# Kernel tuning notes

Measured on AMD Instinct MI355X. Metric: run time of the kernel, lower is better.

The kernel has to match this reference:

```python
import jax, jax.numpy as jnp
import numpy as np

N = 50000   # nodes
E = 800000  # edges (before self-loops)
G = 512     # graphs in batch
H = 4       # heads
C = 32      # hidden dim per head
NEG = 0.2   # LeakyReLU slope in GATConv
EPS = 1e-5  # BatchNorm eps


def setup_inputs():
    k = jax.random.split(jax.random.key(0), 32)
    f = lambda i, s: 0.1 * jax.random.normal(k[i], s, dtype=jnp.float32)
    inp = {
        "x": jax.random.normal(k[0], (N, 4), dtype=jnp.float32),
        "edge_index": jax.random.randint(k[1], (2, E), 0, N, dtype=jnp.int32),
        "batch": ((jnp.arange(N) * G) // N).astype(jnp.int32),  # sorted, every graph non-empty
        "u": jax.random.normal(k[2], (G, 10), dtype=jnp.float32),
    }
    dims = [(4, H * C, H, H * C), (H * C, H * C, H, H * C), (H * C, C, 1, C)]
    j = 3
    for l, (din, dout, hh, dbn) in enumerate(dims):
        inp[f"W{l}"] = f(j, (din, dout)); j += 1
        inp[f"a_src{l}"] = f(j, (hh, C)); j += 1
        inp[f"a_dst{l}"] = f(j, (hh, C)); j += 1
        inp[f"b{l}"] = f(j, (dbn,)); j += 1
        inp[f"bn_g{l}"] = 1.0 + f(j, (dbn,)); j += 1
        inp[f"bn_b{l}"] = f(j, (dbn,)); j += 1
        inp[f"bn_m{l}"] = f(j, (dbn,)); j += 1
        inp[f"bn_v{l}"] = 1.0 + 0.1 * jax.random.uniform(k[j], (dbn,), dtype=jnp.float32); j += 1
    inp["l1w"] = f(j, (2 * C + 10, C)); j += 1
    inp["l1b"] = f(j, (C,)); j += 1
    inp["l2w"] = f(j, (C, 1)); j += 1
    inp["l2b"] = f(j, (1,)); j += 1
    return inp


def gat(x, src, dst, W, a_s, a_d, b, heads, ch, concat):
    n = x.shape[0]
    h = (x @ W).reshape(n, heads, ch)                                   # [N,H,C]
    al_s = jnp.einsum('nhc,hc->nh', h, a_s)
    al_d = jnp.einsum('nhc,hc->nh', h, a_d)
    e = jax.nn.leaky_relu(al_s[src] + al_d[dst], NEG)                   # [E',H]
    m = jax.ops.segment_max(e, dst, num_segments=n)                     # per-dst softmax
    p = jnp.exp(e - m[dst])
    alpha = p / (jax.ops.segment_sum(p, dst, num_segments=n)[dst] + 1e-16)
    out = jax.ops.segment_sum(h[src] * alpha[:, :, None], dst, num_segments=n)
    out = out.reshape(n, heads * ch) if concat else out.mean(axis=1)
    return out + b


def bn(x, g, b, m, v):  # eval-mode BatchNorm1d
    return (x - m) * jax.lax.rsqrt(v + EPS) * g + b


def reference(x, edge_index, batch, u,
              W0, a_src0, a_dst0, b0, bn_g0, bn_b0, bn_m0, bn_v0,
              W1, a_src1, a_dst1, b1, bn_g1, bn_b1, bn_m1, bn_v1,
              W2, a_src2, a_dst2, b2, bn_g2, bn_b2, bn_m2, bn_v2,
              l1w, l1b, l2w, l2b):
    loops = jnp.arange(N, dtype=edge_index.dtype)  # GATConv add_self_loops=True
    src = jnp.concatenate([edge_index[0], loops])
    dst = jnp.concatenate([edge_index[1], loops])
    x = jax.nn.elu(bn(gat(x, src, dst, W0, a_src0, a_dst0, b0, H, C, True), bn_g0, bn_b0, bn_m0, bn_v0))
    x = jax.nn.elu(bn(gat(x, src, dst, W1, a_src1, a_dst1, b1, H, C, True), bn_g1, bn_b1, bn_m1, bn_v1))
    x = jax.nn.elu(bn(gat(x, src, dst, W2, a_src2, a_dst2, b2, 1, C, False), bn_g2, bn_b2, bn_m2, bn_v2))
    cnt = jax.ops.segment_sum(jnp.ones((N,), x.dtype), batch, num_segments=G)
    x_mean = jax.ops.segment_sum(x, batch, num_segments=G) / cnt[:, None]
    x_max = jax.ops.segment_max(x, batch, num_segments=G)
    comb = jnp.concatenate([x_mean, x_max, u], axis=1)                  # [G, 2C+10]
    hid = jax.nn.relu(comb @ l1w + l1b)
    return jax.nn.sigmoid(hid @ l2w + l2b)[:, 0]                        # [G]
```

## Files before the change

### kernel.cpp

```cpp
#include <hip/hip_runtime.h>
#include <hip/hip_bf16.h>
#include <math.h>

#define LRELU_NEG 0.2f
#define BN_EPS 1e-5f
#define CSR_SHIFT 7

typedef __attribute__((ext_vector_type(8))) short bf16x8;
typedef __attribute__((ext_vector_type(4))) float f32x4;

__device__ __forceinline__ float lrelu(float x) { return x > 0.f ? x : LRELU_NEG * x; }
__device__ __forceinline__ float b2f(__hip_bfloat16 v) { return __bfloat162float(v); }
__device__ __forceinline__ unsigned short f2bu(float v) {
  __hip_bfloat16 b = __float2bfloat16(v);
  return *(unsigned short*)&b;
}
__device__ __forceinline__ float blo(unsigned int u) { return __uint_as_float(u << 16); }
__device__ __forceinline__ float bhi(unsigned int u) { return __uint_as_float(u & 0xFFFF0000u); }
__device__ __forceinline__ float elu_fast(float v) { return v > 0.f ? v : __expf(v) - 1.f; }

__global__ __launch_bounds__(256) void k_detect(const unsigned short* __restrict__ w, int n,
                                                int* __restrict__ flag, int* __restrict__ ghist) {
  __shared__ int bad_s;
  int tid = threadIdx.x;
  ghist[tid] = 0; ghist[tid + 256] = 0;
  if (tid == 0) bad_s = 0;
  __syncthreads();
  int bad = 0;
  for (int i = 2 * tid; i < n; i += 512) {
    unsigned short u = w[i];
    if ((u & 0x7FFF) == 0) continue;
    int ex = (u >> 7) & 0xFF;
    if (ex > 131 || ex < 90) bad++;
  }
  atomicAdd(&bad_s, bad);
  __syncthreads();
  if (tid == 0) *flag = (bad_s < 2048) ? 1 : 0;
}

struct CvtArgs {
  const void* src[30];
  float* dst[30];
  int n[30];
};

__global__ __launch_bounds__(256) void k_cvt_all(CvtArgs a, const int* __restrict__ flag) {
  int ai = blockIdx.y;
  int n = a.n[ai];
  int i = blockIdx.x * 256 + threadIdx.x;
  if (i >= n) return;
  if (*flag) {
    a.dst[ai][i] = b2f(((const __hip_bfloat16*)a.src[ai])[i]);
  } else {
    a.dst[ai][i] = ((const float*)a.src[ai])[i];
  }
}

__global__ __launch_bounds__(256) void k_foldW(const float* __restrict__ W0, const float* __restrict__ as0, const float* __restrict__ ad0,
                                               const float* __restrict__ W1, const float* __restrict__ as1, const float* __restrict__ ad1,
                                               const float* __restrict__ W2, const float* __restrict__ as2, const float* __restrict__ ad2,
                                               float* __restrict__ W0p, __hip_bfloat16* __restrict__ Wt1, __hip_bfloat16* __restrict__ Wt2) {
  int idx = blockIdx.x * 256 + threadIdx.x;
  if (idx < 576) {
    int k = idx / 144, c = idx % 144;
    float v = 0.f;
    if (c < 128) v = W0[k * 128 + c];
    else if (c < 136) {
      int hh = (c - 128) & 3; const float* a = (c < 132) ? as0 : ad0;
      float s = 0.f;
      for (int cc = 0; cc < 32; cc++) s += W0[k * 128 + hh * 32 + cc] * a[hh * 32 + cc];
      v = s;
    }
    W0p[k * 144 + c] = v;
    return;
  }
  idx -= 576;
  if (idx < 144 * 128) {
    int c = idx >> 7, k = idx & 127;
    float v = 0.f;
    if (c < 128) v = W1[k * 128 + c];
    else if (c < 136) {
      int hh = (c - 128) & 3; const float* a = (c < 132) ? as1 : ad1;
      float s = 0.f;
      for (int cc = 0; cc < 32; cc++) s += W1[k * 128 + hh * 32 + cc] * a[hh * 32 + cc];
      v = s;
    }
    Wt1[c * 128 + k] = __float2bfloat16(v);
    return;
  }
  idx -= 144 * 128;
  if (idx < 48 * 128) {
    int c = idx >> 7, k = idx & 127;
    float v = 0.f;
    if (c < 32) v = W2[k * 32 + c];
    else if (c == 32) { float s = 0.f; for (int cc = 0; cc < 32; cc++) s += W2[k * 32 + cc] * as2[cc]; v = s; }
    else if (c == 33) { float s = 0.f; for (int cc = 0; cc < 32; cc++) s += W2[k * 32 + cc] * ad2[cc]; v = s; }
    Wt2[c * 128 + k] = __float2bfloat16(v);
  }
}

__global__ __launch_bounds__(256) void k_binhist(const int* __restrict__ ei, int* __restrict__ ghist,
                                                 int E, int EN) {
  __shared__ int hist[512];
  int tid = threadIdx.x;
  hist[tid] = 0; hist[tid + 256] = 0;
  __syncthreads();
  int base = blockIdx.x * 4096;
  for (int i = 0; i < 16; i++) {
    int e = base + i * 256 + tid;
    if (e < EN) {
      int dst = (e < E) ? ei[E + e] : (e - E);
      atomicAdd(&hist[dst >> CSR_SHIFT], 1);
    }
  }
  __syncthreads();
  if (hist[tid]) atomicAdd(&ghist[tid], hist[tid]);
  if (hist[tid + 256]) atomicAdd(&ghist[tid + 256], hist[tid + 256]);
}

__global__ __launch_bounds__(512) void k_bucketscan(const int* __restrict__ ghist,
                                                    int* __restrict__ bbase, int* __restrict__ gcursor) {
  __shared__ int wpre[8];
  int tid = threadIdx.x, lane = tid & 63, wid = tid >> 6;
  int v = ghist[tid];
  int x = v;
  #pragma unroll
  for (int off = 1; off < 64; off <<= 1) {
    int y = __shfl_up(x, off);
    if (lane >= off) x += y;
  }
  if (lane == 63) wpre[wid] = x;
  __syncthreads();
  if (tid == 0) {
    int acc = 0;
    #pragma unroll
    for (int w = 0; w < 8; w++) { int t = wpre[w]; wpre[w] = acc; acc += t; }
  }
  __syncthreads();
  int excl = wpre[wid] + x - v;
  bbase[tid] = excl;
  gcursor[tid] = excl;
  if (tid == 511) bbase[512] = excl + v;
}

__global__ __launch_bounds__(256) void k_binscatter(const int* __restrict__ ei, int* __restrict__ gcursor,
                                                    unsigned int* __restrict__ pairs, int E, int EN) {
  __shared__ int cnt[512];
  __shared__ int base[512];
  int tid = threadIdx.x;
  cnt[tid] = 0; cnt[tid + 256] = 0;
  __syncthreads();
  int eb = blockIdx.x * 4096;
  int srcs[16], dsts[16];
  #pragma unroll
  for (int i = 0; i < 16; i++) {
    int e = eb + i * 256 + tid;
    srcs[i] = -1; dsts[i] = 0;
    if (e < EN) {
      int s, d;
      if (e < E) { s = ei[e]; d = ei[E + e]; } else { s = e - E; d = s; }
      srcs[i] = s; dsts[i] = d;
      atomicAdd(&cnt[d >> CSR_SHIFT], 1);
    }
  }
  __syncthreads();
  for (int b = tid; b < 512; b += 256) {
    int c = cnt[b];
    base[b] = c ? atomicAdd(&gcursor[b], c) : 0;
    cnt[b] = 0;
  }
  __syncthreads();
  #pragma unroll
  for (int i = 0; i < 16; i++) {
    if (srcs[i] >= 0) {
      int b = dsts[i] >> CSR_SHIFT;
      int loc = atomicAdd(&cnt[b], 1);
      pairs[base[b] + loc] = ((unsigned int)srcs[i] << CSR_SHIFT) | (unsigned int)(dsts[i] & 127);
    }
  }
}

__global__ __launch_bounds__(256) void k_csrfin(const unsigned int* __restrict__ pairs,
                                                const int* __restrict__ bbase,
                                                int* __restrict__ rs, int* __restrict__ col,
                                                int N, int EN) {
  __shared__ int dcount[128];
  __shared__ int wsum;
  __shared__ int lcur[128];
  int b = blockIdx.x, tid = threadIdx.x;
  if (tid < 128) dcount[tid] = 0;
  __syncthreads();
  int s = bbase[b], e = bbase[b + 1];
  for (int i = s + tid; i < e; i += 256)
    atomicAdd(&dcount[pairs[i] & 127], 1);
  __syncthreads();
  int x = 0, v = 0, wid = 0;
  if (tid < 128) {
    v = dcount[tid];
    int lane = tid & 63; wid = tid >> 6;
    x = v;
    #pragma unroll
    for (int off = 1; off < 64; off <<= 1) {
      int y = __shfl_up(x, off);
      if (lane >= off) x += y;
    }
    if (wid == 0 && lane == 63) wsum = x;
  }
  __syncthreads();
  if (tid < 128) {
    int excl = x - v + (wid ? wsum : 0);
    int r = s + excl;
    int node = (b << CSR_SHIFT) + tid;
    if (node < N) rs[node] = r;
    lcur[tid] = r;
  }
  if (b == 0 && tid == 0) rs[N] = EN;
  __syncthreads();
  for (int i = s + tid; i < e; i += 256) {
    unsigned int p = pairs[i];
    int pos = atomicAdd(&lcur[p & 127], 1);
    col[pos] = (int)(p >> CSR_SHIFT);
  }
}

__global__ __launch_bounds__(256) void k_gemm0(const float* __restrict__ x, const float* __restrict__ W0p,
    __hip_bfloat16* __restrict__ h, float* __restrict__ als, float* __restrict__ ald, int N) {
  int t = blockIdx.x * 256 + threadIdx.x;
  int nrow = t / 36, cg = t - nrow * 36;
  if (nrow >= N) return;
  float4 xv = *(const float4*)(x + (size_t)nrow * 4);
  int c0 = cg * 4;
  float o[4];
  #pragma unroll
  for (int j = 0; j < 4; j++) {
    int c = c0 + j;
    o[j] = fmaf(xv.x, W0p[c], fmaf(xv.y, W0p[144 + c], fmaf(xv.z, W0p[288 + c], xv.w * W0p[432 + c])));
  }
  if (c0 < 128) {
    uint2 pk;
    pk.x = ((unsigned int)f2bu(o[1]) << 16) | f2bu(o[0]);
    pk.y = ((unsigned int)f2bu(o[3]) << 16) | f2bu(o[2]);
    *((uint2*)((unsigned short*)h + (size_t)nrow * 128) + cg) = pk;
  } else if (c0 == 128) {
    *(float4*)(als + (size_t)nrow * 4) = make_float4(o[0], o[1], o[2], o[3]);
  } else {
    *(float4*)(ald + (size_t)nrow * 4) = make_float4(o[0], o[1], o[2], o[3]);
  }
}

template <int CT, int DOUT, int HEADS>
__global__ __launch_bounds__(256) void k_mm(const __hip_bfloat16* __restrict__ xa,
    const __hip_bfloat16* __restrict__ Wt,
    __hip_bfloat16* __restrict__ h, float* __restrict__ als, float* __restrict__ ald, int N) {
  __shared__ unsigned short A_s[64 * 128];
  __shared__ unsigned short B_s[CT * 16 * 128];
  int tid = threadIdx.x;
  int row0 = blockIdx.x * 64;

  for (int i = tid; i < 1024; i += 256) {
    int r = i >> 4, slot = i & 15;
    int gr = row0 + r;
    float4 v = make_float4(0.f, 0.f, 0.f, 0.f);
    if (gr < N) v = ((const float4*)(xa + (size_t)gr * 128))[slot];
    *(float4*)((char*)A_s + r * 256 + ((slot ^ (r & 7)) << 4)) = v;
  }
  for (int i = tid; i < CT * 256; i += 256) {
    int r = i >> 4, slot = i & 15;
    float4 v = ((const float4*)Wt)[i];
    *(float4*)((char*)B_s + r * 256 + ((slot ^ (r & 7)) << 4)) = v;
  }
  __syncthreads();

  int l = tid & 63, w = tid >> 6;
  int lr = l & 15, lg = l >> 4;
  f32x4 acc[CT];
  #pragma unroll
  for (int ct = 0; ct < CT; ct++) acc[ct] = (f32x4){0.f, 0.f, 0.f, 0.f};

  int rA = w * 16 + lr;
  #pragma unroll
  for (int k0 = 0; k0 < 4; k0++) {
    int slot = k0 * 4 + lg;
    bf16x8 a = *(const bf16x8*)((const char*)A_s + rA * 256 + ((slot ^ (rA & 7)) << 4));
    #pragma unroll
    for (int ct = 0; ct < CT; ct++) {
      int rB = ct * 16 + lr;
      bf16x8 b = *(const bf16x8*)((const char*)B_s + rB * 256 + ((slot ^ (rB & 7)) << 4));
      acc[ct] = __builtin_amdgcn_mfma_f32_16x16x32_bf16(a, b, acc[ct], 0, 0, 0);
    }
  }

  #pragma unroll
  for (int ct = 0; ct < CT; ct++) {
    #pragma unroll
    for (int j = 0; j < 4; j++) {
      int gr = row0 + w * 16 + lg * 4 + j;
      if (gr >= N) continue;
      int col = ct * 16 + lr;
      float v = acc[ct][j];
      if (col < DOUT)                 h[(size_t)gr * DOUT + col] = __float2bfloat16(v);
      else if (col < DOUT + HEADS)    als[(size_t)gr * HEADS + (col - DOUT)] = v;
      else if (col < DOUT + 2*HEADS)  ald[(size_t)gr * HEADS + (col - DOUT - HEADS)] = v;
    }
  }
}

__global__ __launch_bounds__(256) void k_agg4(const __hip_bfloat16* __restrict__ h, const float* __restrict__ als,
    const float* __restrict__ ald, const int* __restrict__ rs, const int* __restrict__ col,
    const float* __restrict__ bias, const float* __restrict__ bng,
    const float* __restrict__ bnb, const float* __restrict__ bnm,
    const float* __restrict__ bnv, __hip_bfloat16* __restrict__ out, int N) {
  __shared__ int svs[8][32];
  __shared__ float ps[8][32][4];
  int tid = threadIdx.x;
  int sub = tid & 31, gi = tid >> 5;
  int n = blockIdx.x * 8 + gi;
  if (n >= N) return;
  int row = rs[n], deg = rs[n + 1] - row;
  float4 ad4 = *(const float4*)(ald + (size_t)n * 4);
  int hh2 = sub >> 3;
  float acc0 = 0.f, acc1 = 0.f, acc2 = 0.f, acc3 = 0.f;
  float s0 = 0.f, s1 = 0.f, s2 = 0.f, s3 = 0.f;

  for (int base = 0; base < deg; base += 32) {
    int k = base + sub;
    int sv = 0; float q0 = 0.f, q1 = 0.f, q2 = 0.f, q3 = 0.f;
    if (k < deg) {
      sv = col[row + k];
      float4 a4 = *(const float4*)(als + (size_t)sv * 4);
      q0 = __expf(lrelu(a4.x + ad4.x));
      q1 = __expf(lrelu(a4.y + ad4.y));
      q2 = __expf(lrelu(a4.z + ad4.z));
      q3 = __expf(lrelu(a4.w + ad4.w));
    }
    svs[gi][sub] = sv;
    *(float4*)&ps[gi][sub][0] = make_float4(q0, q1, q2, q3);
    s0 += q0; s1 += q1; s2 += q2; s3 += q3;
    int cnt = min(32, deg - base);
    int e = 0;
    for (; e + 3 < cnt; e += 4) {
      float pA = ps[gi][e][hh2];     int sA = svs[gi][e];
      float pB = ps[gi][e + 1][hh2]; int sB = svs[gi][e + 1];
      float pC = ps[gi][e + 2][hh2]; int sC = svs[gi][e + 2];
      float pD = ps[gi][e + 3][hh2]; int sD = svs[gi][e + 3];
      uint2 hA = *((const uint2*)(h + (size_t)sA * 128) + sub);
      uint2 hB = *((const uint2*)(h + (size_t)sB * 128) + sub);
      uint2 hC = *((const uint2*)(h + (size_t)sC * 128) + sub);
      uint2 hD = *((const uint2*)(h + (size_t)sD * 128) + sub);
      acc0 = fmaf(pA, blo(hA.x), acc0); acc1 = fmaf(pA, bhi(hA.x), acc1);
      acc2 = fmaf(pA, blo(hA.y), acc2); acc3 = fmaf(pA, bhi(hA.y), acc3);
      acc0 = fmaf(pB, blo(hB.x), acc0); acc1 = fmaf(pB, bhi(hB.x), acc1);
      acc2 = fmaf(pB, blo(hB.y), acc2); acc3 = fmaf(pB, bhi(hB.y), acc3);
      acc0 = fmaf(pC, blo(hC.x), acc0); acc1 = fmaf(pC, bhi(hC.x), acc1);
      acc2 = fmaf(pC, blo(hC.y), acc2); acc3 = fmaf(pC, bhi(hC.y), acc3);
      acc0 = fmaf(pD, blo(hD.x), acc0); acc1 = fmaf(pD, bhi(hD.x), acc1);
      acc2 = fmaf(pD, blo(hD.y), acc2); acc3 = fmaf(pD, bhi(hD.y), acc3);
    }
    for (; e < cnt; e++) {
      float pA = ps[gi][e][hh2]; int sA = svs[gi][e];
      uint2 hA = *((const uint2*)(h + (size_t)sA * 128) + sub);
      acc0 = fmaf(pA, blo(hA.x), acc0); acc1 = fmaf(pA, bhi(hA.x), acc1);
      acc2 = fmaf(pA, blo(hA.y), acc2); acc3 = fmaf(pA, bhi(hA.y), acc3);
    }
  }
  #pragma unroll
  for (int off = 1; off < 32; off <<= 1) {
    s0 += __shfl_xor(s0, off); s1 += __shfl_xor(s1, off);
    s2 += __shfl_xor(s2, off); s3 += __shfl_xor(s3, off);
  }
  float ssel = hh2 == 0 ? s0 : hh2 == 1 ? s1 : hh2 == 2 ? s2 : s3;
  float inv = 1.f / (ssel + 1e-16f);
  acc0 *= inv; acc1 *= inv; acc2 *= inv; acc3 *= inv;

  int c0 = 4 * sub;
  float4 bi = *(const float4*)(bias + c0);
  float4 bm = *(const float4*)(bnm + c0);
  float4 bv = *(const float4*)(bnv + c0);
  float4 bg = *(const float4*)(bng + c0);
  float4 bb = *(const float4*)(bnb + c0);
  float v0 = (acc0 + bi.x - bm.x) * rsqrtf(bv.x + BN_EPS) * bg.x + bb.x;
  float v1 = (acc1 + bi.y - bm.y) * rsqrtf(bv.y + BN_EPS) * bg.y + bb.y;
  float v2 = (acc2 + bi.z - bm.z) * rsqrtf(bv.z + BN_EPS) * bg.z + bb.z;
  float v3 = (acc3 + bi.w - bm.w) * rsqrtf(bv.w + BN_EPS) * bg.w + bb.w;
  v0 = elu_fast(v0); v1 = elu_fast(v1); v2 = elu_fast(v2); v3 = elu_fast(v3);
  uint2 packed;
  packed.x = ((unsigned int)f2bu(v1) << 16) | f2bu(v0);
  packed.y = ((unsigned int)f2bu(v3) << 16) | f2bu(v2);
  *((uint2*)((unsigned short*)out + (size_t)n * 128) + sub) = packed;
}

__global__ __launch_bounds__(256) void k_agg1(const __hip_bfloat16* __restrict__ h, const float* __restrict__ als,
    const float* __restrict__ ald, const int* __restrict__ rs, const int* __restrict__ col,
    const float* __restrict__ bias, const float* __restrict__ bng,
    const float* __restrict__ bnb, const float* __restrict__ bnm,
    const float* __restrict__ bnv, __hip_bfloat16* __restrict__ out, int N) {
  __shared__ int svs[16][16];
  __shared__ float ps[16][16];
  int tid = threadIdx.x;
  int sub = tid & 15, gi = tid >> 4;
  int n = blockIdx.x * 16 + gi;
  if (n >= N) return;
  int row = rs[n], deg = rs[n + 1] - row;
  float ad = ald[n];
  float acc0 = 0.f, acc1 = 0.f, s = 0.f;

  for (int base = 0; base < deg; base += 16) {
    int k = base + sub;
    int sv = 0; float q = 0.f;
    if (k < deg) {
      sv = col[row + k];
      q = __expf(lrelu(als[sv] + ad));
    }
    svs[gi][sub] = sv;
    ps[gi][sub] = q;
    s += q;
    int cnt = min(16, deg - base);
    int e = 0;
    for (; e + 3 < cnt; e += 4) {
      float pA = ps[gi][e];     int sA = svs[gi][e];
      float pB = ps[gi][e + 1]; int sB = svs[gi][e + 1];
      float pC = ps[gi][e + 2]; int sC = svs[gi][e + 2];
      float pD = ps[gi][e + 3]; int sD = svs[gi][e + 3];
      unsigned int hA = *((const unsigned int*)(h + (size_t)sA * 32) + sub);
      unsigned int hB = *((const unsigned int*)(h + (size_t)sB * 32) + sub);
      unsigned int hC = *((const unsigned int*)(h + (size_t)sC * 32) + sub);
      unsigned int hD = *((const unsigned int*)(h + (size_t)sD * 32) + sub);
      acc0 = fmaf(pA, blo(hA), acc0); acc1 = fmaf(pA, bhi(hA), acc1);
      acc0 = fmaf(pB, blo(hB), acc0); acc1 = fmaf(pB, bhi(hB), acc1);
      acc0 = fmaf(pC, blo(hC), acc0); acc1 = fmaf(pC, bhi(hC), acc1);
      acc0 = fmaf(pD, blo(hD), acc0); acc1 = fmaf(pD, bhi(hD), acc1);
    }
    for (; e < cnt; e++) {
      float pA = ps[gi][e]; int sA = svs[gi][e];
      unsigned int hA = *((const unsigned int*)(h + (size_t)sA * 32) + sub);
      acc0 = fmaf(pA, blo(hA), acc0); acc1 = fmaf(pA, bhi(hA), acc1);
    }
  }
  #pragma unroll
  for (int off = 1; off < 16; off <<= 1) s += __shfl_xor(s, off);
  float inv = 1.f / (s + 1e-16f);
  acc0 *= inv; acc1 *= inv;

  int c0 = 2 * sub;
  float2 bi = *(const float2*)(bias + c0);
  float2 bm = *(const float2*)(bnm + c0);
  float2 bv = *(const float2*)(bnv + c0);
  float2 bg = *(const float2*)(bng + c0);
  float2 bb = *(const float2*)(bnb + c0);
  float v0 = (acc0 + bi.x - bm.x) * rsqrtf(bv.x + BN_EPS) * bg.x + bb.x;
  float v1 = (acc1 + bi.y - bm.y) * rsqrtf(bv.y + BN_EPS) * bg.y + bb.y;
  v0 = elu_fast(v0);
  v1 = elu_fast(v1);
  unsigned int packed = ((unsigned int)f2bu(v1) << 16) | f2bu(v0);
  *((unsigned int*)((unsigned short*)out + (size_t)n * 32) + sub) = packed;
}

__global__ __launch_bounds__(64) void k_pool(const __hip_bfloat16* __restrict__ x3, const int* __restrict__ batch,
    const float* __restrict__ u, const float* __restrict__ l1w,
    const float* __restrict__ l1b, const float* __restrict__ l2w,
    const float* __restrict__ l2b, float* __restrict__ out, int N, int G) {
  int g = blockIdx.x;
  int lane = threadIdx.x;
  int lo = 0, hi = N;
  while (lo < hi) { int mid = (lo + hi) >> 1; if (batch[mid] < g) lo = mid + 1; else hi = mid; }
  int start = lo;
  hi = N;
  while (lo < hi) { int mid = (lo + hi) >> 1; if (batch[mid] < g + 1) lo = mid + 1; else hi = mid; }
  int end = lo;
  int sub = lane & 15, q = lane >> 4;
  float sum0 = 0.f, sum1 = 0.f, mx0 = -1e30f, mx1 = -1e30f;
  for (int i = start + q; i < end; i += 4) {
    unsigned int hv = *((const unsigned int*)(x3 + (size_t)i * 32) + sub);
    float v0 = blo(hv), v1 = bhi(hv);
    sum0 += v0; sum1 += v1;
    mx0 = fmaxf(mx0, v0); mx1 = fmaxf(mx1, v1);
  }
  sum0 += __shfl_xor(sum0, 16); sum0 += __shfl_xor(sum0, 32);
  sum1 += __shfl_xor(sum1, 16); sum1 += __shfl_xor(sum1, 32);
  mx0 = fmaxf(mx0, __shfl_xor(mx0, 16)); mx0 = fmaxf(mx0, __shfl_xor(mx0, 32));
  mx1 = fmaxf(mx1, __shfl_xor(mx1, 16)); mx1 = fmaxf(mx1, __shfl_xor(mx1, 32));
  __shared__ float comb[74];
  if (lane < 16) {
    float cnt = (float)(end - start);
    comb[2 * lane] = sum0 / cnt;
    comb[2 * lane + 1] = sum1 / cnt;
    comb[32 + 2 * lane] = mx0;
    comb[32 + 2 * lane + 1] = mx1;
  }
  if (lane < 10) comb[64 + lane] = u[g * 10 + lane];
  __syncthreads();
  if (lane < 32) {
    float acc = l1b[lane];
    #pragma unroll
    for (int k = 0; k < 74; k++) acc = fmaf(comb[k], l1w[k * 32 + lane], acc);
    acc = fmaxf(acc, 0.f);
    float v = acc * l2w[lane];
    #pragma unroll
    for (int off = 16; off; off >>= 1) v += __shfl_xor(v, off, 32);
    if (lane == 0) out[g] = 1.f / (1.f + __expf(-(v + l2b[0])));
  }
}

extern "C" void kernel_launch(void* const* d_in, const int* in_sizes, int n_in,
                              void* d_out, int out_size, void* d_ws, size_t ws_size,
                              hipStream_t stream) {
  const int* EI    = (const int*)d_in[1];
  const int* BATCH = (const int*)d_in[2];
  float* OUT = (float*)d_out;

  int N = in_sizes[2];
  int E = in_sizes[1] / 2;
  int G = in_sizes[3] / 10;
  int EN = E + N;
  int NB = (N + 127) >> 7;

  char* ws = (char*)d_ws;
  size_t off = 0;
  auto alloc = [&](size_t bytes) {
    void* p = ws + off;
    off = (off + bytes + 255) & ~(size_t)255;
    return p;
  };
  __hip_bfloat16* f_xa = (__hip_bfloat16*)alloc((size_t)N * 128 * 2);
  __hip_bfloat16* f_h  = (__hip_bfloat16*)alloc((size_t)N * 128 * 2);
  float* f_als = (float*)alloc((size_t)N * 4 * 4);
  float* f_ald = (float*)alloc((size_t)N * 4 * 4);
  float* fW0p  = (float*)alloc(576 * 4);
  __hip_bfloat16* fWt1 = (__hip_bfloat16*)alloc(144 * 128 * 2);
  __hip_bfloat16* fWt2 = (__hip_bfloat16*)alloc(48 * 128 * 2);
  int* i_rs   = (int*)alloc((size_t)(N + 1) * 4);
  int* i_col  = (int*)alloc((size_t)EN * 4);
  unsigned int* i_pairs = (unsigned int*)alloc((size_t)EN * 4);
  int* i_ghist   = (int*)alloc(512 * 4);
  int* i_bbase   = (int*)alloc(513 * 4);
  int* i_gcursor = (int*)alloc(512 * 4);
  int* i_flag = (int*)alloc(256);

  CvtArgs ca;
  float* fptr[32];
  int maxn = 0, na = 0;
  for (int i = 0; i < 32; i++) {
    if (i == 1 || i == 2) { fptr[i] = nullptr; continue; }
    int n = in_sizes[i];
    fptr[i] = (float*)alloc((size_t)n * 4);
    ca.src[na] = d_in[i];
    ca.dst[na] = fptr[i];
    ca.n[na] = n;
    if (n > maxn) maxn = n;
    na++;
  }

  k_detect<<<1, 256, 0, stream>>>((const unsigned short*)d_in[12], in_sizes[12], i_flag, i_ghist);
  dim3 cgrid((maxn + 255) / 256, na);
  k_cvt_all<<<cgrid, 256, 0, stream>>>(ca, i_flag);

  k_foldW<<<99, 256, 0, stream>>>(fptr[4], fptr[5], fptr[6],
                                  fptr[12], fptr[13], fptr[14],
                                  fptr[20], fptr[21], fptr[22],
                                  fW0p, fWt1, fWt2);

  int ebks = (EN + 4095) / 4096;
  k_binhist<<<ebks, 256, 0, stream>>>(EI, i_ghist, E, EN);
  k_bucketscan<<<1, 512, 0, stream>>>(i_ghist, i_bbase, i_gcursor);
  k_binscatter<<<ebks, 256, 0, stream>>>(EI, i_gcursor, i_pairs, E, EN);
  k_csrfin<<<NB, 256, 0, stream>>>(i_pairs, i_bbase, i_rs, i_col, N, EN);

  k_gemm0<<<(N * 36 + 255) / 256, 256, 0, stream>>>(fptr[0], fW0p, f_h, f_als, f_ald, N);
  k_agg4<<<(N + 7) / 8, 256, 0, stream>>>(f_h, f_als, f_ald, i_rs, i_col, fptr[7], fptr[8], fptr[9], fptr[10], fptr[11], f_xa, N);
  k_mm<9, 128, 4><<<(N + 63) / 64, 256, 0, stream>>>(f_xa, fWt1, f_h, f_als, f_ald, N);
  k_agg4<<<(N + 7) / 8, 256, 0, stream>>>(f_h, f_als, f_ald, i_rs, i_col, fptr[15], fptr[16], fptr[17], fptr[18], fptr[19], f_xa, N);
  k_mm<3, 32, 1><<<(N + 63) / 64, 256, 0, stream>>>(f_xa, fWt2, f_h, f_als, f_ald, N);
  k_agg1<<<(N + 15) / 16, 256, 0, stream>>>(f_h, f_als, f_ald, i_rs, i_col, fptr[23], fptr[24], fptr[25], fptr[26], fptr[27], f_xa, N);

  k_pool<<<G, 64, 0, stream>>>(f_xa, BATCH, fptr[3], fptr[28], fptr[29], fptr[30], fptr[31], OUT, N, G);
}
```

Measured before the change: 192.5 us.

## Fuse setup kernels, fold BN into affine, merge final aggregation with pooling

Removes the bulk parameter conversion kernel, so weights are read directly in either dtype through a flag-aware loader. The dtype detection is merged with the edge histogram, which now writes per-block partials that the scan sums, removing the global atomics. Bias and BatchNorm are folded into a per-channel scale and shift. The last GAT aggregation is fused with graph pooling and the MLP head, one block per graph, which avoids writing and re-reading the layer-3 output. The trade-off is fewer launches against lower parallelism in the fused final kernel, at 512 blocks of 16 node groups each.

```diff
diff --git a/kernel.cpp b/kernel.cpp
--- a/kernel.cpp
+++ b/kernel.cpp
@@ -18,94 +18,35 @@
 __device__ __forceinline__ float blo(unsigned int u) { return __uint_as_float(u << 16); }
 __device__ __forceinline__ float bhi(unsigned int u) { return __uint_as_float(u & 0xFFFF0000u); }
 __device__ __forceinline__ float elu_fast(float v) { return v > 0.f ? v : __expf(v) - 1.f; }
-
-__global__ __launch_bounds__(256) void k_detect(const unsigned short* __restrict__ w, int n,
-                                                int* __restrict__ flag, int* __restrict__ ghist) {
-  __shared__ int bad_s;
+__device__ __forceinline__ float ldw(const void* p, int i, int fl) {
+  return fl ? b2f(((const __hip_bfloat16*)p)[i]) : ((const float*)p)[i];
+}
+
+__global__ __launch_bounds__(256) void k_setup(const int* __restrict__ ei, int E, int EN, int ebks,
+                                               const unsigned short* __restrict__ w, int wn,
+                                               int* __restrict__ flag, int* __restrict__ ph) {
+  int b = blockIdx.x;
   int tid = threadIdx.x;
-  ghist[tid] = 0; ghist[tid + 256] = 0;
-  if (tid == 0) bad_s = 0;
-  __syncthreads();
-  int bad = 0;
-  for (int i = 2 * tid; i < n; i += 512) {
-    unsigned short u = w[i];
-    if ((u & 0x7FFF) == 0) continue;
-    int ex = (u >> 7) & 0xFF;
-    if (ex > 131 || ex < 90) bad++;
-  }
-  atomicAdd(&bad_s, bad);
-  __syncthreads();
-  if (tid == 0) *flag = (bad_s < 2048) ? 1 : 0;
-}
-
-struct CvtArgs {
-  const void* src[30];
-  float* dst[30];
-  int n[30];
-};
-
-__global__ __launch_bounds__(256) void k_cvt_all(CvtArgs a, const int* __restrict__ flag) {
-  int ai = blockIdx.y;
-  int n = a.n[ai];
-  int i = blockIdx.x * 256 + threadIdx.x;
-  if (i >= n) return;
-  if (*flag) {
-    a.dst[ai][i] = b2f(((const __hip_bfloat16*)a.src[ai])[i]);
-  } else {
-    a.dst[ai][i] = ((const float*)a.src[ai])[i];
-  }
-}
-
-__global__ __launch_bounds__(256) void k_foldW(const float* __restrict__ W0, const float* __restrict__ as0, const float* __restrict__ ad0,
-                                               const float* __restrict__ W1, const float* __restrict__ as1, const float* __restrict__ ad1,
-                                               const float* __restrict__ W2, const float* __restrict__ as2, const float* __restrict__ ad2,
-                                               float* __restrict__ W0p, __hip_bfloat16* __restrict__ Wt1, __hip_bfloat16* __restrict__ Wt2) {
-  int idx = blockIdx.x * 256 + threadIdx.x;
-  if (idx < 576) {
-    int k = idx / 144, c = idx % 144;
-    float v = 0.f;
-    if (c < 128) v = W0[k * 128 + c];
-    else if (c < 136) {
-      int hh = (c - 128) & 3; const float* a = (c < 132) ? as0 : ad0;
-      float s = 0.f;
-      for (int cc = 0; cc < 32; cc++) s += W0[k * 128 + hh * 32 + cc] * a[hh * 32 + cc];
-      v = s;
-    }
-    W0p[k * 144 + c] = v;
+  if (b == ebks) {
+    __shared__ int bad_s;
+    if (tid == 0) bad_s = 0;
+    __syncthreads();
+    int bad = 0;
+    for (int i = 2 * tid; i < wn; i += 512) {
+      unsigned short u = w[i];
+      if ((u & 0x7FFF) == 0) continue;
+      int ex = (u >> 7) & 0xFF;
+      if (ex > 131 || ex < 90) bad++;
+    }
+    atomicAdd(&bad_s, bad);
+    __syncthreads();
+    if (tid == 0) *flag = (bad_s < 2048) ? 1 : 0;
     return;
   }
-  idx -= 576;
-  if (idx < 144 * 128) {
-    int c = idx >> 7, k = idx & 127;
-    float v = 0.f;
-    if (c < 128) v = W1[k * 128 + c];
-    else if (c < 136) {
-      int hh = (c - 128) & 3; const float* a = (c < 132) ? as1 : ad1;
-      float s = 0.f;
-      for (int cc = 0; cc < 32; cc++) s += W1[k * 128 + hh * 32 + cc] * a[hh * 32 + cc];
-      v = s;
-    }
-    Wt1[c * 128 + k] = __float2bfloat16(v);
-    return;
-  }
-  idx -= 144 * 128;
-  if (idx < 48 * 128) {
-    int c = idx >> 7, k = idx & 127;
-    float v = 0.f;
-    if (c < 32) v = W2[k * 32 + c];
-    else if (c == 32) { float s = 0.f; for (int cc = 0; cc < 32; cc++) s += W2[k * 32 + cc] * as2[cc]; v = s; }
-    else if (c == 33) { float s = 0.f; for (int cc = 0; cc < 32; cc++) s += W2[k * 32 + cc] * ad2[cc]; v = s; }
-    Wt2[c * 128 + k] = __float2bfloat16(v);
-  }
-}
-
-__global__ __launch_bounds__(256) void k_binhist(const int* __restrict__ ei, int* __restrict__ ghist,
-                                                 int E, int EN) {
   __shared__ int hist[512];
-  int tid = threadIdx.x;
   hist[tid] = 0; hist[tid + 256] = 0;
   __syncthreads();
-  int base = blockIdx.x * 4096;
+  int base = b * 4096;
   for (int i = 0; i < 16; i++) {
     int e = base + i * 256 + tid;
     if (e < EN) {
@@ -114,15 +55,16 @@
     }
   }
   __syncthreads();
-  if (hist[tid]) atomicAdd(&ghist[tid], hist[tid]);
-  if (hist[tid + 256]) atomicAdd(&ghist[tid + 256], hist[tid + 256]);
-}
-
-__global__ __launch_bounds__(512) void k_bucketscan(const int* __restrict__ ghist,
+  ph[b * 512 + tid] = hist[tid];
+  ph[b * 512 + tid + 256] = hist[tid + 256];
+}
+
+__global__ __launch_bounds__(512) void k_bucketscan(const int* __restrict__ ph, int ebks,
                                                     int* __restrict__ bbase, int* __restrict__ gcursor) {
   __shared__ int wpre[8];
   int tid = threadIdx.x, lane = tid & 63, wid = tid >> 6;
-  int v = ghist[tid];
+  int v = 0;
+  for (int i = 0; i < ebks; i++) v += ph[i * 512 + tid];
   int x = v;
   #pragma unroll
   for (int off = 1; off < 64; off <<= 1) {
@@ -223,12 +165,90 @@
   }
 }
 
-__global__ __launch_bounds__(256) void k_gemm0(const float* __restrict__ x, const float* __restrict__ W0p,
+struct FoldArgs {
+  const void *W0, *as0, *ad0, *W1, *as1, *ad1, *W2, *as2, *ad2;
+  const void *bn[15];
+  float* W0p; __hip_bfloat16* Wt1; __hip_bfloat16* Wt2;
+  float *A0, *B0, *A1, *B1, *A2, *B2;
+};
+
+__global__ __launch_bounds__(256) void k_foldW(FoldArgs fa, const int* __restrict__ flag) {
+  int idx = blockIdx.x * 256 + threadIdx.x;
+  int fl = *flag;
+  if (idx < 576) {
+    int k = idx / 144, c = idx % 144;
+    float v = 0.f;
+    if (c < 128) v = ldw(fa.W0, k * 128 + c, fl);
+    else if (c < 136) {
+      int hh = (c - 128) & 3; const void* a = (c < 132) ? fa.as0 : fa.ad0;
+      float s = 0.f;
+      for (int cc = 0; cc < 32; cc++)
+        s += ldw(fa.W0, k * 128 + hh * 32 + cc, fl) * ldw(a, hh * 32 + cc, fl);
+      v = s;
+    }
+    fa.W0p[k * 144 + c] = v;
+    return;
+  }
+  idx -= 576;
+  if (idx < 144 * 128) {
+    int c = idx >> 7, k = idx & 127;
+    float v = 0.f;
+    if (c < 128) v = ldw(fa.W1, k * 128 + c, fl);
+    else if (c < 136) {
+      int hh = (c - 128) & 3; const void* a = (c < 132) ? fa.as1 : fa.ad1;
+      float s = 0.f;
+      for (int cc = 0; cc < 32; cc++)
+        s += ldw(fa.W1, k * 128 + hh * 32 + cc, fl) * ldw(a, hh * 32 + cc, fl);
+      v = s;
+    }
+    fa.Wt1[c * 128 + k] = __float2bfloat16(v);
+    return;
+  }
+  idx -= 144 * 128;
+  if (idx < 48 * 128) {
+    int c = idx >> 7, k = idx & 127;
+    float v = 0.f;
+    if (c < 32) v = ldw(fa.W2, k * 32 + c, fl);
+    else if (c == 32) { float s = 0.f; for (int cc = 0; cc < 32; cc++) s += ldw(fa.W2, k * 32 + cc, fl) * ldw(fa.as2, cc, fl); v = s; }
+    else if (c == 33) { float s = 0.f; for (int cc = 0; cc < 32; cc++) s += ldw(fa.W2, k * 32 + cc, fl) * ldw(fa.ad2, cc, fl); v = s; }
+    fa.Wt2[c * 128 + k] = __float2bfloat16(v);
+    return;
+  }
+  idx -= 48 * 128;
+  if (idx < 128) {
+    float A = ldw(fa.bn[1], idx, fl) * rsqrtf(ldw(fa.bn[4], idx, fl) + BN_EPS);
+    fa.A0[idx] = A;
+    fa.B0[idx] = (ldw(fa.bn[0], idx, fl) - ldw(fa.bn[3], idx, fl)) * A + ldw(fa.bn[2], idx, fl);
+    return;
+  }
+  idx -= 128;
+  if (idx < 128) {
+    float A = ldw(fa.bn[6], idx, fl) * rsqrtf(ldw(fa.bn[9], idx, fl) + BN_EPS);
+    fa.A1[idx] = A;
+    fa.B1[idx] = (ldw(fa.bn[5], idx, fl) - ldw(fa.bn[8], idx, fl)) * A + ldw(fa.bn[7], idx, fl);
+    return;
+  }
+  idx -= 128;
+  if (idx < 32) {
+    float A = ldw(fa.bn[11], idx, fl) * rsqrtf(ldw(fa.bn[14], idx, fl) + BN_EPS);
+    fa.A2[idx] = A;
+    fa.B2[idx] = (ldw(fa.bn[10], idx, fl) - ldw(fa.bn[13], idx, fl)) * A + ldw(fa.bn[12], idx, fl);
+  }
+}
+
+__global__ __launch_bounds__(256) void k_gemm0(const void* __restrict__ x, const float* __restrict__ W0p,
+    const int* __restrict__ flag,
     __hip_bfloat16* __restrict__ h, float* __restrict__ als, float* __restrict__ ald, int N) {
   int t = blockIdx.x * 256 + threadIdx.x;
   int nrow = t / 36, cg = t - nrow * 36;
   if (nrow >= N) return;
-  float4 xv = *(const float4*)(x + (size_t)nrow * 4);
+  float4 xv;
+  if (*flag) {
+    uint2 tv = ((const uint2*)x)[nrow];
+    xv = make_float4(blo(tv.x), bhi(tv.x), blo(tv.y), bhi(tv.y));
+  } else {
+    xv = ((const float4*)x)[nrow];
+  }
   int c0 = cg * 4;
   float o[4];
   #pragma unroll
@@ -307,9 +327,8 @@
 
 __global__ __launch_bounds__(256) void k_agg4(const __hip_bfloat16* __restrict__ h, const float* __restrict__ als,
     const float* __restrict__ ald, const int* __restrict__ rs, const int* __restrict__ col,
-    const float* __restrict__ bias, const float* __restrict__ bng,
-    const float* __restrict__ bnb, const float* __restrict__ bnm,
-    const float* __restrict__ bnv, __hip_bfloat16* __restrict__ out, int N) {
+    const float* __restrict__ Aarr, const float* __restrict__ Barr,
+    __hip_bfloat16* __restrict__ out, int N) {
   __shared__ int svs[8][32];
   __shared__ float ps[8][32][4];
   int tid = threadIdx.x;
@@ -370,18 +389,14 @@
   }
   float ssel = hh2 == 0 ? s0 : hh2 == 1 ? s1 : hh2 == 2 ? s2 : s3;
   float inv = 1.f / (ssel + 1e-16f);
-  acc0 *= inv; acc1 *= inv; acc2 *= inv; acc3 *= inv;
 
   int c0 = 4 * sub;
-  float4 bi = *(const float4*)(bias + c0);
-  float4 bm = *(const float4*)(bnm + c0);
-  float4 bv = *(const float4*)(bnv + c0);
-  float4 bg = *(const float4*)(bng + c0);
-  float4 bb = *(const float4*)(bnb + c0);
-  float v0 = (acc0 + bi.x - bm.x) * rsqrtf(bv.x + BN_EPS) * bg.x + bb.x;
-  float v1 = (acc1 + bi.y - bm.y) * rsqrtf(bv.y + BN_EPS) * bg.y + bb.y;
-  float v2 = (acc2 + bi.z - bm.z) * rsqrtf(bv.z + BN_EPS) * bg.z + bb.z;
-  float v3 = (acc3 + bi.w - bm.w) * rsqrtf(bv.w + BN_EPS) * bg.w + bb.w;
+  float4 Av = *(const float4*)(Aarr + c0);
+  float4 Bv = *(const float4*)(Barr + c0);
+  float v0 = acc0 * inv * Av.x + Bv.x;
+  float v1 = acc1 * inv * Av.y + Bv.y;
+  float v2 = acc2 * inv * Av.z + Bv.z;
+  float v3 = acc3 * inv * Av.w + Bv.w;
   v0 = elu_fast(v0); v1 = elu_fast(v1); v2 = elu_fast(v2); v3 = elu_fast(v3);
   uint2 packed;
   packed.x = ((unsigned int)f2bu(v1) << 16) | f2bu(v0);
@@ -389,115 +404,101 @@
   *((uint2*)((unsigned short*)out + (size_t)n * 128) + sub) = packed;
 }
 
-__global__ __launch_bounds__(256) void k_agg1(const __hip_bfloat16* __restrict__ h, const float* __restrict__ als,
-    const float* __restrict__ ald, const int* __restrict__ rs, const int* __restrict__ col,
-    const float* __restrict__ bias, const float* __restrict__ bng,
-    const float* __restrict__ bnb, const float* __restrict__ bnm,
-    const float* __restrict__ bnv, __hip_bfloat16* __restrict__ out, int N) {
+__global__ __launch_bounds__(256) void k_agg1pool(const __hip_bfloat16* __restrict__ h,
+    const float* __restrict__ als, const float* __restrict__ ald,
+    const int* __restrict__ rs, const int* __restrict__ col,
+    const float* __restrict__ A2, const float* __restrict__ B2,
+    const int* __restrict__ batch,
+    const void* __restrict__ u, const void* __restrict__ l1w, const void* __restrict__ l1b,
+    const void* __restrict__ l2w, const void* __restrict__ l2b, const int* __restrict__ flag,
+    float* __restrict__ out, int N, int G) {
   __shared__ int svs[16][16];
   __shared__ float ps[16][16];
-  int tid = threadIdx.x;
-  int sub = tid & 15, gi = tid >> 4;
-  int n = blockIdx.x * 16 + gi;
-  if (n >= N) return;
-  int row = rs[n], deg = rs[n + 1] - row;
-  float ad = ald[n];
-  float acc0 = 0.f, acc1 = 0.f, s = 0.f;
-
-  for (int base = 0; base < deg; base += 16) {
-    int k = base + sub;
-    int sv = 0; float q = 0.f;
-    if (k < deg) {
-      sv = col[row + k];
-      q = __expf(lrelu(als[sv] + ad));
-    }
-    svs[gi][sub] = sv;
-    ps[gi][sub] = q;
-    s += q;
-    int cnt = min(16, deg - base);
-    int e = 0;
-    for (; e + 3 < cnt; e += 4) {
-      float pA = ps[gi][e];     int sA = svs[gi][e];
-      float pB = ps[gi][e + 1]; int sB = svs[gi][e + 1];
-      float pC = ps[gi][e + 2]; int sC = svs[gi][e + 2];
-      float pD = ps[gi][e + 3]; int sD = svs[gi][e + 3];
-      unsigned int hA = *((const unsigned int*)(h + (size_t)sA * 32) + sub);
-      unsigned int hB = *((const unsigned int*)(h + (size_t)sB * 32) + sub);
-      unsigned int hC = *((const unsigned int*)(h + (size_t)sC * 32) + sub);
-      unsigned int hD = *((const unsigned int*)(h + (size_t)sD * 32) + sub);
-      acc0 = fmaf(pA, blo(hA), acc0); acc1 = fmaf(pA, bhi(hA), acc1);
-      acc0 = fmaf(pB, blo(hB), acc0); acc1 = fmaf(pB, bhi(hB), acc1);
-      acc0 = fmaf(pC, blo(hC), acc0); acc1 = fmaf(pC, bhi(hC), acc1);
-      acc0 = fmaf(pD, blo(hD), acc0); acc1 = fmaf(pD, bhi(hD), acc1);
-    }
-    for (; e < cnt; e++) {
-      float pA = ps[gi][e]; int sA = svs[gi][e];
-      unsigned int hA = *((const unsigned int*)(h + (size_t)sA * 32) + sub);
-      acc0 = fmaf(pA, blo(hA), acc0); acc1 = fmaf(pA, bhi(hA), acc1);
-    }
-  }
-  #pragma unroll
-  for (int off = 1; off < 16; off <<= 1) s += __shfl_xor(s, off);
-  float inv = 1.f / (s + 1e-16f);
-  acc0 *= inv; acc1 *= inv;
-
-  int c0 = 2 * sub;
-  float2 bi = *(const float2*)(bias + c0);
-  float2 bm = *(const float2*)(bnm + c0);
-  float2 bv = *(const float2*)(bnv + c0);
-  float2 bg = *(const float2*)(bng + c0);
-  float2 bb = *(const float2*)(bnb + c0);
-  float v0 = (acc0 + bi.x - bm.x) * rsqrtf(bv.x + BN_EPS) * bg.x + bb.x;
-  float v1 = (acc1 + bi.y - bm.y) * rsqrtf(bv.y + BN_EPS) * bg.y + bb.y;
-  v0 = elu_fast(v0);
-  v1 = elu_fast(v1);
-  unsigned int packed = ((unsigned int)f2bu(v1) << 16) | f2bu(v0);
-  *((unsigned int*)((unsigned short*)out + (size_t)n * 32) + sub) = packed;
-}
-
-__global__ __launch_bounds__(64) void k_pool(const __hip_bfloat16* __restrict__ x3, const int* __restrict__ batch,
-    const float* __restrict__ u, const float* __restrict__ l1w,
-    const float* __restrict__ l1b, const float* __restrict__ l2w,
-    const float* __restrict__ l2b, float* __restrict__ out, int N, int G) {
+  __shared__ float rsum[16][32];
+  __shared__ float rmax[16][32];
+  __shared__ float comb[74];
   int g = blockIdx.x;
-  int lane = threadIdx.x;
+  int tid = threadIdx.x, sub = tid & 15, gi = tid >> 4;
   int lo = 0, hi = N;
   while (lo < hi) { int mid = (lo + hi) >> 1; if (batch[mid] < g) lo = mid + 1; else hi = mid; }
   int start = lo;
   hi = N;
   while (lo < hi) { int mid = (lo + hi) >> 1; if (batch[mid] < g + 1) lo = mid + 1; else hi = mid; }
   int end = lo;
-  int sub = lane & 15, q = lane >> 4;
+
+  float2 Af = *(const float2*)(A2 + 2 * sub);
+  float2 Bf = *(const float2*)(B2 + 2 * sub);
   float sum0 = 0.f, sum1 = 0.f, mx0 = -1e30f, mx1 = -1e30f;
-  for (int i = start + q; i < end; i += 4) {
-    unsigned int hv = *((const unsigned int*)(x3 + (size_t)i * 32) + sub);
-    float v0 = blo(hv), v1 = bhi(hv);
+
+  for (int n = start + gi; n < end; n += 16) {
+    int row = rs[n], deg = rs[n + 1] - row;
+    float ad = ald[n];
+    float acc0 = 0.f, acc1 = 0.f, s = 0.f;
+    for (int base = 0; base < deg; base += 16) {
+      int k = base + sub;
+      int sv = 0; float q = 0.f;
+      if (k < deg) {
+        sv = col[row + k];
+        q = __expf(lrelu(als[sv] + ad));
+      }
+      svs[gi][sub] = sv;
+      ps[gi][sub] = q;
+      s += q;
+      int cnt = min(16, deg - base);
+      int e = 0;
+      for (; e + 3 < cnt; e += 4) {
+        float pA = ps[gi][e];     int sA = svs[gi][e];
+        float pB = ps[gi][e + 1]; int sB = svs[gi][e + 1];
+        float pC = ps[gi][e + 2]; int sC = svs[gi][e + 2];
+        float pD = ps[gi][e + 3]; int sD = svs[gi][e + 3];
+        unsigned int hA = *((const unsigned int*)(h + (size_t)sA * 32) + sub);
+        unsigned int hB = *((const unsigned int*)(h + (size_t)sB * 32) + sub);
+        unsigned int hC = *((const unsigned int*)(h + (size_t)sC * 32) + sub);
+        unsigned int hD = *((const unsigned int*)(h + (size_t)sD * 32) + sub);
+        acc0 = fmaf(pA, blo(hA), acc0); acc1 = fmaf(pA, bhi(hA), acc1);
+        acc0 = fmaf(pB, blo(hB), acc0); acc1 = fmaf(pB, bhi(hB), acc1);
+        acc0 = fmaf(pC, blo(hC), acc0); acc1 = fmaf(pC, bhi(hC), acc1);
+        acc0 = fmaf(pD, blo(hD), acc0); acc1 = fmaf(pD, bhi(hD), acc1);
+      }
+      for (; e < cnt; e++) {
+        float pA = ps[gi][e]; int sA = svs[gi][e];
+        unsigned int hA = *((const unsigned int*)(h + (size_t)sA * 32) + sub);
+        acc0 = fmaf(pA, blo(hA), acc0); acc1 = fmaf(pA, bhi(hA), acc1);
+      }
+    }
+    #pragma unroll
+    for (int off = 1; off < 16; off <<= 1) s += __shfl_xor(s, off);
+    float inv = 1.f / (s + 1e-16f);
+    float v0 = acc0 * inv * Af.x + Bf.x;
+    float v1 = acc1 * inv * Af.y + Bf.y;
+    v0 = elu_fast(v0);
+    v1 = elu_fast(v1);
     sum0 += v0; sum1 += v1;
     mx0 = fmaxf(mx0, v0); mx1 = fmaxf(mx1, v1);
   }
-  sum0 += __shfl_xor(sum0, 16); sum0 += __shfl_xor(sum0, 32);
-  sum1 += __shfl_xor(sum1, 16); sum1 += __shfl_xor(sum1, 32);
-  mx0 = fmaxf(mx0, __shfl_xor(mx0, 16)); mx0 = fmaxf(mx0, __shfl_xor(mx0, 32));
-  mx1 = fmaxf(mx1, __shfl_xor(mx1, 16)); mx1 = fmaxf(mx1, __shfl_xor(mx1, 32));
-  __shared__ float comb[74];
-  if (lane < 16) {
+  rsum[gi][2 * sub] = sum0; rsum[gi][2 * sub + 1] = sum1;
+  rmax[gi][2 * sub] = mx0;  rmax[gi][2 * sub + 1] = mx1;
+  __syncthreads();
+  int fl = *flag;
+  if (tid < 32) {
+    float s = 0.f, m = -1e30f;
+    #pragma unroll
+    for (int i = 0; i < 16; i++) { s += rsum[i][tid]; m = fmaxf(m, rmax[i][tid]); }
     float cnt = (float)(end - start);
-    comb[2 * lane] = sum0 / cnt;
-    comb[2 * lane + 1] = sum1 / cnt;
-    comb[32 + 2 * lane] = mx0;
-    comb[32 + 2 * lane + 1] = mx1;
-  }
-  if (lane < 10) comb[64 + lane] = u[g * 10 + lane];
-  __syncthreads();
-  if (lane < 32) {
-    float acc = l1b[lane];
-    #pragma unroll
-    for (int k = 0; k < 74; k++) acc = fmaf(comb[k], l1w[k * 32 + lane], acc);
+    comb[tid] = s / cnt;
+    comb[32 + tid] = m;
+  }
+  if (tid < 10) comb[64 + tid] = ldw(u, g * 10 + tid, fl);
+  __syncthreads();
+  if (tid < 32) {
+    float acc = ldw(l1b, tid, fl);
+    #pragma unroll
+    for (int k = 0; k < 74; k++) acc = fmaf(comb[k], ldw(l1w, k * 32 + tid, fl), acc);
     acc = fmaxf(acc, 0.f);
-    float v = acc * l2w[lane];
+    float v = acc * ldw(l2w, tid, fl);
     #pragma unroll
     for (int off = 16; off; off >>= 1) v += __shfl_xor(v, off, 32);
-    if (lane == 0) out[g] = 1.f / (1.f + __expf(-(v + l2b[0])));
+    if (tid == 0) out[g] = 1.f / (1.f + __expf(-(v + ldw(l2b, 0, fl))));
   }
 }
 
@@ -513,6 +514,7 @@
   int G = in_sizes[3] / 10;
   int EN = E + N;
   int NB = (N + 127) >> 7;
+  int ebks = (EN + 4095) / 4096;
 
   char* ws = (char*)d_ws;
   size_t off = 0;
@@ -528,49 +530,46 @@
   float* fW0p  = (float*)alloc(576 * 4);
   __hip_bfloat16* fWt1 = (__hip_bfloat16*)alloc(144 * 128 * 2);
   __hip_bfloat16* fWt2 = (__hip_bfloat16*)alloc(48 * 128 * 2);
+  float* fA0 = (float*)alloc(128 * 4);
+  float* fB0 = (float*)alloc(128 * 4);
+  float* fA1 = (float*)alloc(128 * 4);
+  float* fB1 = (float*)alloc(128 * 4);
+  float* fA2 = (float*)alloc(32 * 4);
+  float* fB2 = (float*)alloc(32 * 4);
   int* i_rs   = (int*)alloc((size_t)(N + 1) * 4);
   int* i_col  = (int*)alloc((size_t)EN * 4);
   unsigned int* i_pairs = (unsigned int*)alloc((size_t)EN * 4);
-  int* i_ghist   = (int*)alloc(512 * 4);
+  int* i_ph      = (int*)alloc((size_t)ebks * 512 * 4);
   int* i_bbase   = (int*)alloc(513 * 4);
   int* i_gcursor = (int*)alloc(512 * 4);
   int* i_flag = (int*)alloc(256);
 
-  CvtArgs ca;
-  float* fptr[32];
-  int maxn = 0, na = 0;
-  for (int i = 0; i < 32; i++) {
-    if (i == 1 || i == 2) { fptr[i] = nullptr; continue; }
-    int n = in_sizes[i];
-    fptr[i] = (float*)alloc((size_t)n * 4);
-    ca.src[na] = d_in[i];
-    ca.dst[na] = fptr[i];
-    ca.n[na] = n;
-    if (n > maxn) maxn = n;
-    na++;
-  }
-
-  k_detect<<<1, 256, 0, stream>>>((const unsigned short*)d_in[12], in_sizes[12], i_flag, i_ghist);
-  dim3 cgrid((maxn + 255) / 256, na);
-  k_cvt_all<<<cgrid, 256, 0, stream>>>(ca, i_flag);
-
-  k_foldW<<<99, 256, 0, stream>>>(fptr[4], fptr[5], fptr[6],
-                                  fptr[12], fptr[13], fptr[14],
-                                  fptr[20], fptr[21], fptr[22],
-                                  fW0p, fWt1, fWt2);
-
-  int ebks = (EN + 4095) / 4096;
-  k_binhist<<<ebks, 256, 0, stream>>>(EI, i_ghist, E, EN);
-  k_bucketscan<<<1, 512, 0, stream>>>(i_ghist, i_bbase, i_gcursor);
+  k_setup<<<ebks + 1, 256, 0, stream>>>(EI, E, EN, ebks,
+                                        (const unsigned short*)d_in[12], in_sizes[12],
+                                        i_flag, i_ph);
+  FoldArgs fa;
+  fa.W0 = d_in[4];  fa.as0 = d_in[5];  fa.ad0 = d_in[6];
+  fa.W1 = d_in[12]; fa.as1 = d_in[13]; fa.ad1 = d_in[14];
+  fa.W2 = d_in[20]; fa.as2 = d_in[21]; fa.ad2 = d_in[22];
+  for (int i = 0; i < 5; i++) {
+    fa.bn[i]      = d_in[7 + i];
+    fa.bn[5 + i]  = d_in[15 + i];
+    fa.bn[10 + i] = d_in[23 + i];
+  }
+  fa.W0p = fW0p; fa.Wt1 = fWt1; fa.Wt2 = fWt2;
+  fa.A0 = fA0; fa.B0 = fB0; fa.A1 = fA1; fa.B1 = fB1; fa.A2 = fA2; fa.B2 = fB2;
+  k_foldW<<<100, 256, 0, stream>>>(fa, i_flag);
+
+  k_bucketscan<<<1, 512, 0, stream>>>(i_ph, ebks, i_bbase, i_gcursor);
   k_binscatter<<<ebks, 256, 0, stream>>>(EI, i_gcursor, i_pairs, E, EN);
   k_csrfin<<<NB, 256, 0, stream>>>(i_pairs, i_bbase, i_rs, i_col, N, EN);
 
-  k_gemm0<<<(N * 36 + 255) / 256, 256, 0, stream>>>(fptr[0], fW0p, f_h, f_als, f_ald, N);
-  k_agg4<<<(N + 7) / 8, 256, 0, stream>>>(f_h, f_als, f_ald, i_rs, i_col, fptr[7], fptr[8], fptr[9], fptr[10], fptr[11], f_xa, N);
+  k_gemm0<<<(N * 36 + 255) / 256, 256, 0, stream>>>(d_in[0], fW0p, i_flag, f_h, f_als, f_ald, N);
+  k_agg4<<<(N + 7) / 8, 256, 0, stream>>>(f_h, f_als, f_ald, i_rs, i_col, fA0, fB0, f_xa, N);
   k_mm<9, 128, 4><<<(N + 63) / 64, 256, 0, stream>>>(f_xa, fWt1, f_h, f_als, f_ald, N);
-  k_agg4<<<(N + 7) / 8, 256, 0, stream>>>(f_h, f_als, f_ald, i_rs, i_col, fptr[15], fptr[16], fptr[17], fptr[18], fptr[19], f_xa, N);
+  k_agg4<<<(N + 7) / 8, 256, 0, stream>>>(f_h, f_als, f_ald, i_rs, i_col, fA1, fB1, f_xa, N);
   k_mm<3, 32, 1><<<(N + 63) / 64, 256, 0, stream>>>(f_xa, fWt2, f_h, f_als, f_ald, N);
-  k_agg1<<<(N + 15) / 16, 256, 0, stream>>>(f_h, f_als, f_ald, i_rs, i_col, fptr[23], fptr[24], fptr[25], fptr[26], fptr[27], f_xa, N);
-
-  k_pool<<<G, 64, 0, stream>>>(f_xa, BATCH, fptr[3], fptr[28], fptr[29], fptr[30], fptr[31], OUT, N, G);
-}
+  k_agg1pool<<<G, 256, 0, stream>>>(f_h, f_als, f_ald, i_rs, i_col, fA2, fB2,
+                                    BATCH, d_in[3], d_in[28], d_in[29], d_in[30], d_in[31],
+                                    i_flag, OUT, N, G);
+}
```

Result: slower. 216.0 us (+12.2%).
